# Kernel tuning notes

Hardware: AMD Instinct MI355X
Metric: run time of the kernel (lower is better)

## Reference

```python
import jax, jax.numpy as jnp
import numpy as np

B = 256
NO_A, NF_A = 64, 4   # class A: n_obj, n_field (all state fields)
NO_B, NF_B = 32, 3   # class B
NS = NF_A + NF_B     # total state fields = 7
DIN, DL, DG, DH = 128, 64, 64, 256
DGE = DG * NF_A + DG * NF_B          # 448 global encoding dim
DIN_A = DGE + DL * NF_A              # 704 decoder input dim, class A
DIN_B = DGE + DL * NF_B              # 640 decoder input dim, class B
NP = 2  # distribution params per field (mean, scale)


def lrelu(x):
    return jnp.where(x >= 0, x, 0.01 * x)


def setup_inputs() -> dict:
    key = jax.random.key(0)
    ks = iter(jax.random.split(key, 40))
    def rn(shape, s=1.0):
        return jax.random.normal(next(ks), shape, jnp.float32) * s
    def w(shape):
        return rn(shape, 0.05)
    def rb(shape):
        return jax.random.randint(next(ks), shape, 0, 2).astype(bool)
    inp = dict(
        x_A=rn((B, NO_A, NF_A, DIN)),
        x_B=rn((B, NO_B, NF_B, DIN)),
        global_mask=rb((B, NS, NF_A + NF_B)),
        local_mask_A=rb((B, NF_A, NF_A)),
        local_mask_B=rb((B, NF_B, NF_B)),
        objmask_A=rb((B, NO_A)),
        objmask_B=rb((B, NO_B)),
        enc_Wl_A=w((DIN, DL)), enc_bl_A=w((DL,)),
        enc_Wg_A=w((DIN, DG)), enc_bg_A=w((DG,)),
        enc_Wl_B=w((DIN, DL)), enc_bl_B=w((DL,)),
        enc_Wg_B=w((DIN, DG)), enc_bg_B=w((DG,)),
        dec_W1_A=w((NF_A, DIN_A, DH)), dec_b1_A=w((NF_A, DH)),
        dec_W2_A=w((NF_A, DH, DH)), dec_b2_A=w((NF_A, DH)),
        dec_Wp_A=w((NF_A, DH, NP)), dec_bp_A=w((NF_A, NP)),
        dec_W1_B=w((NF_B, DIN_B, DH)), dec_b1_B=w((NF_B, DH)),
        dec_W2_B=w((NF_B, DH, DH)), dec_b2_B=w((NF_B, DH)),
        dec_Wp_B=w((NF_B, DH, NP)), dec_bp_B=w((NF_B, NP)),
        rw_W1=w((DGE, DH)), rw_b1=w((DH,)),
        rw_W2=w((DH, DH)), rw_b2=w((DH,)),
        rw_W3=w((DH, 1)), rw_b3=w((1,)),
    )
    return inp


def encode_local(x, Wl, bl, attrmask):
    # x: (B, O, F, DIN) -> (B, O, S, F*DL), masked_retain over attrmask (B, S, F)
    h = jax.nn.relu(x @ Wl + bl)                                  # (B,O,F,DL)
    y = jnp.where(attrmask[:, None, :, :, None], h[:, :, None, :, :], 0.0)  # (B,O,S,F,DL)
    return y.reshape(y.shape[0], y.shape[1], y.shape[2], -1)


def encode_global(x, Wg, bg, attrmask, objmask):
    # x: (B, O, F, DIN), attrmask: (B, NS, F), objmask: (B, O)
    h = x @ Wg + bg                                               # (B,O,F,DG)
    h = jnp.where(objmask[:, :, None, None], h, 0.0)
    r = jax.nn.relu(jnp.sum(h, axis=1))                           # (B,F,DG) sum-pool over objects
    y = jnp.where(attrmask[:, :, :, None], r[:, None], 0.0)       # (B,NS,F,DG)
    y = jnp.concatenate([y, r[:, None]], axis=1)                  # (B,NS+1,F,DG)
    return y.reshape(y.shape[0], y.shape[1], -1)


def decode(x, W1, b1, W2, b2, Wp, bp):
    # x: (B, O, S, Din); per-field (s) decoders stacked on leading axis
    h = lrelu(jnp.einsum('bosi,sid->bosd', x, W1) + b1)
    h = lrelu(jnp.einsum('bosd,sde->bose', h, W2) + b2)
    return jnp.einsum('bose,sep->bosp', h, Wp) + bp               # (B,O,S,NP)


def reference(x_A, x_B, global_mask, local_mask_A, local_mask_B, objmask_A, objmask_B,
              enc_Wl_A, enc_bl_A, enc_Wg_A, enc_bg_A,
              enc_Wl_B, enc_bl_B, enc_Wg_B, enc_bg_B,
              dec_W1_A, dec_b1_A, dec_W2_A, dec_b2_A, dec_Wp_A, dec_bp_A,
              dec_W1_B, dec_b1_B, dec_W2_B, dec_b2_B, dec_Wp_B, dec_bp_B,
              rw_W1, rw_b1, rw_W2, rw_b2, rw_W3, rw_b3):
    g_A = encode_global(x_A, enc_Wg_A, enc_bg_A, global_mask[:, :, :NF_A], objmask_A)
    g_B = encode_global(x_B, enc_Wg_B, enc_bg_B, global_mask[:, :, NF_A:], objmask_B)
    G = jnp.concatenate([g_A, g_B], axis=2)                       # (B, NS+1, DGE)

    l_A = encode_local(x_A, enc_Wl_A, enc_bl_A, local_mask_A)     # (B,NO_A,NF_A,NF_A*DL)
    gs_A = jnp.broadcast_to(G[:, None, :NF_A, :], (B, NO_A, NF_A, DGE))
    out_A = decode(jnp.concatenate([l_A, gs_A], axis=3),
                   dec_W1_A, dec_b1_A, dec_W2_A, dec_b2_A, dec_Wp_A, dec_bp_A)

    l_B = encode_local(x_B, enc_Wl_B, enc_bl_B, local_mask_B)
    gs_B = jnp.broadcast_to(G[:, None, NF_A:NS, :], (B, NO_B, NF_B, DGE))
    out_B = decode(jnp.concatenate([l_B, gs_B], axis=3),
                   dec_W1_B, dec_b1_B, dec_W2_B, dec_b2_B, dec_Wp_B, dec_bp_B)

    h = lrelu(G[:, -1, :] @ rw_W1 + rw_b1)
    h = lrelu(h @ rw_W2 + rw_b2)
    reward = (h @ rw_W3 + rw_b3)[:, 0]                            # (B,)
    return out_A, out_B, reward
```

## Files before the change

kernel.cpp:

```cpp
#include <hip/hip_runtime.h>
#include <hip/hip_bf16.h>

constexpr int Bn   = 256;
constexpr int NOA  = 64, NFA = 4;
constexpr int NOB  = 32, NFB = 3;
constexpr int NS   = 7;
constexpr int DIN  = 128, DL = 64, DG = 64, DH = 256;
constexpr int DGE  = 448;
constexpr int DINA = 704;
constexpr int DINB = 640;

typedef short  short8v __attribute__((ext_vector_type(8)));
typedef float  f32x4   __attribute__((ext_vector_type(4)));

__device__ __forceinline__ unsigned short f2bf(float x) {
  union { float f; unsigned int u; } a; a.f = x;
  unsigned int r = a.u + 0x7fff + ((a.u >> 16) & 1);
  return (unsigned short)(r >> 16);
}


struct MidArgs {
  const float *xA, *xB, *WlA, *WlB, *blA, *blB;
  unsigned short *hlA, *hlB;
  const int *omA, *omB;
  const float *WgA, *bgA, *WgB, *bgB;
  float *rA, *rB;
  const float *W1A, *W1B, *W2A, *W2B;
  unsigned short *W1tA, *W1tB, *W1gtA, *W1gtB, *W2tA, *W2tB;
};

template<int F>
__device__ void hl_body(const float* __restrict__ x, const float* __restrict__ Wl,
                        const float* __restrict__ bl, unsigned short* __restrict__ hlf,
                        int m0, unsigned char* smem) {
  auto Asb = reinterpret_cast<unsigned short(*)[72]>(smem);
  auto Bsb = reinterpret_cast<unsigned short(*)[136]>(smem + 36864);
  float (*tile)[65] = reinterpret_cast<float(*)[65]>(smem);
  const int t = threadIdx.x, w = t >> 6, lane = t & 63;
  const int lr = lane & 15, lg = lane >> 4;
  constexpr int KB1 = 2 * F;

#pragma unroll
  for (int i = 0; i < 32; ++i) {
    int idx = t + i * 256;
    tile[idx >> 6][idx & 63] = Wl[idx];
  }
  __syncthreads();
#pragma unroll
  for (int i = 0; i < 32; ++i) {
    int idx = t + i * 256;
    int n = idx >> 7, k = idx & 127;
    Bsb[n][k] = f2bf(tile[k][n]);
  }
  __syncthreads();

  f32x4 acc[4][4] = {};
  for (int k0 = 0; k0 < DIN; k0 += 64) {
    const float* xp = x + (size_t)(m0 + t) * DIN + k0;
#pragma unroll
    for (int j = 0; j < 8; ++j) {
      float4 a = *(const float4*)(xp + j * 8);
      float4 b = *(const float4*)(xp + j * 8 + 4);
      union { short8v v; unsigned short e[8]; } u;
      u.e[0] = f2bf(a.x); u.e[1] = f2bf(a.y); u.e[2] = f2bf(a.z); u.e[3] = f2bf(a.w);
      u.e[4] = f2bf(b.x); u.e[5] = f2bf(b.y); u.e[6] = f2bf(b.z); u.e[7] = f2bf(b.w);
      *reinterpret_cast<short8v*>(&Asb[t][j * 8]) = u.v;
    }
#pragma unroll
    for (int ks = 0; ks < 2; ++ks) {
      short8v af[4], bf[4];
#pragma unroll
      for (int mi = 0; mi < 4; ++mi)
        af[mi] = *reinterpret_cast<const short8v*>(&Asb[w * 64 + mi * 16 + lr][ks * 32 + lg * 8]);
#pragma unroll
      for (int ni = 0; ni < 4; ++ni)
        bf[ni] = *reinterpret_cast<const short8v*>(&Bsb[ni * 16 + lr][k0 + ks * 32 + lg * 8]);
#pragma unroll
      for (int mi = 0; mi < 4; ++mi)
#pragma unroll
        for (int ni = 0; ni < 4; ++ni)
          acc[mi][ni] = __builtin_amdgcn_mfma_f32_16x16x32_bf16(
              af[mi], bf[ni], acc[mi][ni], 0, 0, 0);
    }
  }
#pragma unroll
  for (int mi = 0; mi < 4; ++mi)
#pragma unroll
    for (int ni = 0; ni < 4; ++ni)
#pragma unroll
      for (int reg = 0; reg < 4; ++reg) {
        int row = mi * 16 + lg * 4 + reg;
        int col = ni * 16 + lr;
        float v = fmaxf(acc[mi][ni][reg] + bl[col], 0.f);
        Asb[w * 64 + row][col] = f2bf(v);
      }
  const int mpb = m0 + w * 64;
#pragma unroll
  for (int j = 0; j < 8; ++j) {
    int c = lane + j * 64;
    int ml = c >> 3, dls = c & 7;
    int mp = mpb + ml;
    int mrow = mp / F, f = mp % F;
    int m6 = mrow >> 6, mi = (mrow >> 4) & 3, lr2 = mrow & 15;
    int kb = 2 * f + (dls >> 2), lg2 = dls & 3;
    size_t dst = ((((size_t)m6 * KB1 + kb) * 4 + mi) * 64 + (lg2 * 16 + lr2)) * 8;
    *reinterpret_cast<short8v*>(hlf + dst) =
        *reinterpret_cast<const short8v*>(&Asb[w * 64 + ml][dls * 8]);
  }
}

template<int O, int F>
__device__ void xsum_rg_body(const float* __restrict__ x, const int* __restrict__ om,
                             const float* __restrict__ Wg, const float* __restrict__ bg,
                             float* __restrict__ r, int b, unsigned char* smem) {
  float* xsm = reinterpret_cast<float*>(smem + 36864 + 17408);
  const int t = threadIdx.x, f = t >> 6, lane = t & 63;
  if (f >= F) return;
  unsigned long long bal = __ballot(lane < O && om[(size_t)b * O + lane] != 0);
  float cnt = (float)__popcll(bal);
  float a0 = 0.f, a1 = 0.f;
  const float* xb = x + ((size_t)b * O * F + f) * DIN + lane;
#pragma unroll 8
  for (int o = 0; o < O; ++o) {
    float m = (float)((bal >> o) & 1ull);
    a0 += m * xb[(size_t)o * F * DIN];
    a1 += m * xb[(size_t)o * F * DIN + 64];
  }
  xsm[f * 128 + lane] = a0;
  xsm[f * 128 + lane + 64] = a1;
  asm volatile("s_waitcnt lgkmcnt(0)" ::: "memory");
  float acc = 0.f;
  const float* wp = Wg + lane;
#pragma unroll 8
  for (int i = 0; i < DIN; ++i) acc += xsm[f * 128 + i] * wp[(size_t)i * DG];
  acc += cnt * bg[lane];
  r[((size_t)b * F + f) * DG + lane] = fmaxf(acc, 0.f);
}

__device__ void wtrans_tile(const float* __restrict__ src, unsigned short* __restrict__ dst,
                            int N, int DINc, int koff, int Kout,
                            int s, int kt, int nt, unsigned char* smem) {
  float (*tile)[65] = reinterpret_cast<float(*)[65]>(smem);
  const int t = threadIdx.x;
#pragma unroll
  for (int i = 0; i < 16; ++i) {
    int rr = (t >> 6) + i * 4, c = t & 63;
    tile[rr][c] = src[((size_t)s * DINc + koff + kt * 64 + rr) * N + nt * 64 + c];
  }
  __syncthreads();
#pragma unroll
  for (int i = 0; i < 2; ++i) {
    int cidx = t + i * 256;
    int n = cidx >> 3, kc = (cidx & 7) * 8;
    union { short8v v; unsigned short e[8]; } u;
#pragma unroll
    for (int j = 0; j < 8; ++j) u.e[j] = f2bf(tile[kc + j][n]);
    *reinterpret_cast<short8v*>(dst + ((size_t)s * N + nt * 64 + n) * Kout + kt * 64 + kc) = u.v;
  }
}

__device__ void wtrans_frag(const float* __restrict__ src, unsigned short* __restrict__ dst,
                            int DINc, int koff, int KB,
                            int s, int kt, int nt, unsigned char* smem) {
  float (*tile)[65] = reinterpret_cast<float(*)[65]>(smem);
  const int t = threadIdx.x;
#pragma unroll
  for (int i = 0; i < 16; ++i) {
    int rr = (t >> 6) + i * 4, c = t & 63;
    tile[rr][c] = src[((size_t)s * DINc + koff + kt * 64 + rr) * 256 + nt * 64 + c];
  }
  __syncthreads();
#pragma unroll
  for (int i = 0; i < 2; ++i) {
    int cidx = t + i * 256;
    int nl = cidx >> 3, kslot = cidx & 7;
    union { short8v v; unsigned short e[8]; } u;
#pragma unroll
    for (int j = 0; j < 8; ++j) u.e[j] = f2bf(tile[kslot * 8 + j][nl]);
    int kb = kt * 2 + (kslot >> 2);
    int lane = (kslot & 3) * 16 + (nl & 15);
    int nchunk = nt * 4 + (nl >> 4);
    *reinterpret_cast<short8v*>(
        dst + ((((size_t)s * KB + kb) * 16 + nchunk) * 64 + lane) * 8) = u.v;
  }
}

__global__ __launch_bounds__(256) void mid_kernel(MidArgs a) {
  __shared__ __align__(16) unsigned char smem[56320];
  const int bid = blockIdx.x;
  if (bid < 256) {
    hl_body<NFA>(a.xA, a.WlA, a.blA, a.hlA, bid * 256, smem);
    xsum_rg_body<NOA, NFA>(a.xA, a.omA, a.WgA, a.bgA, a.rA, bid, smem);
  } else if (bid < 352) {
    hl_body<NFB>(a.xB, a.WlB, a.blB, a.hlB, (bid - 256) * 256, smem);
  } else if (bid < 608) {
    xsum_rg_body<NOB, NFB>(a.xB, a.omB, a.WgB, a.bgB, a.rB, bid - 352, smem);
  } else {
    int r = bid - 608;
    if (r < 64)       { wtrans_frag(a.W1A, a.W1tA, DINA, 0, 8,
                                    r / 16, (r % 16) >> 2, r & 3, smem); }
    else if (r < 100) { r -= 64;  wtrans_frag(a.W1B, a.W1tB, DINB, 0, 6,
                                    r / 12, (r % 12) >> 2, r & 3, smem); }
    else if (r < 212) { r -= 100; wtrans_tile(a.W1A, a.W1gtA, 256, DINA, NFA * DL, DGE,
                                    r / 28, (r % 28) >> 2, r & 3, smem); }
    else if (r < 296) { r -= 212; wtrans_tile(a.W1B, a.W1gtB, 256, DINB, NFB * DL, DGE,
                                    r / 28, (r % 28) >> 2, r & 3, smem); }
    else if (r < 360) { r -= 296; wtrans_frag(a.W2A, a.W2tA, DH, 0, 8,
                                    r / 16, (r % 16) >> 2, r & 3, smem); }
    else              { r -= 360; wtrans_frag(a.W2B, a.W2tB, DH, 0, 8,
                                    r / 16, (r % 16) >> 2, r & 3, smem); }
  }
}

struct GprArgs {
  const float *rA, *rB; const int *gm;
  const unsigned short *W1gtA, *W1gtB;
  const float *b1A, *b1B;
  float *g1A, *g1B;
  const float *rwW1, *rwb1, *rwW2, *rwb2, *rwW3, *rwb3;
  float *outR;
};

__device__ void gpart_body(const GprArgs& a, int bx, int sg, unsigned char* smem) {
  auto Asb = reinterpret_cast<unsigned short(*)[72]>(smem);
  auto Bsb = reinterpret_cast<unsigned short(*)[72]>(smem + 9216);
  const int t = threadIdx.x, w = t >> 6, lane = t & 63;
  const int lr = lane & 15, lg = lane >> 4;
  const int m0 = bx * 64;
  const unsigned short* W1gt; const float* b1; float* g1; int S, sl;
  if (sg < NFA) { W1gt = a.W1gtA; b1 = a.b1A; g1 = a.g1A; S = NFA; sl = sg; }
  else          { W1gt = a.W1gtB; b1 = a.b1B; g1 = a.g1B; S = NFB; sl = sg - NFA; }

  f32x4 acc[4][4] = {};
  for (int kt = 0; kt < 7; ++kt) {
    __syncthreads();
    const int f = kt;
    const float* rsrc = (f < NFA) ? (a.rA + (size_t)f * DG) : (a.rB + (size_t)(f - NFA) * DG);
    const int rstride = (f < NFA) ? NFA * DG : NFB * DG;
#pragma unroll
    for (int i = 0; i < 2; ++i) {
      int c = t + i * 256;
      int row = c >> 3, kc = (c & 7) * 8;
      int b = m0 + row;
      float mk = (a.gm[((size_t)b * NS + sg) * NS + f] != 0) ? 1.f : 0.f;
      const float* rp = rsrc + (size_t)b * rstride + kc;
      union { short8v v; unsigned short e[8]; } u;
#pragma unroll
      for (int j = 0; j < 8; ++j) u.e[j] = f2bf(mk * rp[j]);
      *reinterpret_cast<short8v*>(&Asb[row][kc]) = u.v;
    }
#pragma unroll
    for (int i = 0; i < 8; ++i) {
      int c = t + i * 256;
      int n = c >> 3, kc = (c & 7) * 8;
      *reinterpret_cast<short8v*>(&Bsb[n][kc]) = *reinterpret_cast<const short8v*>(
          W1gt + ((size_t)sl * 256 + n) * DGE + kt * 64 + kc);
    }
    __syncthreads();
#pragma unroll
    for (int ks = 0; ks < 2; ++ks) {
      short8v af[4], bf[4];
#pragma unroll
      for (int mi = 0; mi < 4; ++mi)
        af[mi] = *reinterpret_cast<const short8v*>(&Asb[mi * 16 + lr][ks * 32 + lg * 8]);
#pragma unroll
      for (int ni = 0; ni < 4; ++ni)
        bf[ni] = *reinterpret_cast<const short8v*>(&Bsb[w * 64 + ni * 16 + lr][ks * 32 + lg * 8]);
#pragma unroll
      for (int mi = 0; mi < 4; ++mi)
#pragma unroll
        for (int ni = 0; ni < 4; ++ni)
          acc[mi][ni] = __builtin_amdgcn_mfma_f32_16x16x32_bf16(
              af[mi], bf[ni], acc[mi][ni], 0, 0, 0);
    }
  }
#pragma unroll
  for (int mi = 0; mi < 4; ++mi)
#pragma unroll
    for (int reg = 0; reg < 4; ++reg) {
      int b = m0 + mi * 16 + lg * 4 + reg;
#pragma unroll
      for (int ni = 0; ni < 4; ++ni) {
        int col = w * 64 + ni * 16 + lr;
        g1[((size_t)b * S + sl) * DH + col] = acc[mi][ni][reg] + b1[(size_t)sl * DH + col];
      }
    }
}

__device__ void reward_body(const GprArgs& a, int b, unsigned char* smem) {
  float* Gs = reinterpret_cast<float*>(smem);
  float* h1 = Gs + DGE;
  float* red = h1 + DH;
  const int t = threadIdx.x;
  for (int j = t; j < DGE; j += 256)
    Gs[j] = (j < NFA * DG) ? a.rA[((size_t)b * NFA + (j >> 6)) * DG + (j & 63)]
                           : a.rB[((size_t)b * NFB + ((j - NFA * DG) >> 6)) * DG + (j & 63)];
  __syncthreads();
  float acc = a.rwb1[t];
  for (int j = 0; j < DGE; ++j) acc += Gs[j] * a.rwW1[(size_t)j * DH + t];
  h1[t] = (acc >= 0.f) ? acc : 0.01f * acc;
  __syncthreads();
  acc = a.rwb2[t];
  for (int j = 0; j < DH; ++j) acc += h1[j] * a.rwW2[(size_t)j * DH + t];
  acc = (acc >= 0.f) ? acc : 0.01f * acc;
  red[t] = acc * a.rwW3[t];
  __syncthreads();
  for (int off = 128; off > 0; off >>= 1) {
    if (t < off) red[t] += red[t + off];
    __syncthreads();
  }
  if (t == 0) a.outR[b] = red[0] + a.rwb3[0];
}

__global__ __launch_bounds__(256) void gpr_kernel(GprArgs a) {
  __shared__ __align__(16) unsigned char smem[46080];
  const int bid = blockIdx.x;
  if (bid < 28) gpart_body(a, bid & 3, bid >> 2, smem);
  else          reward_body(a, bid - 28, smem);
}

struct DecArgs {
  const unsigned short *hlA, *hlB, *W1tA, *W1tB, *W2tA, *W2tB;
  const int *lmA, *lmB;
  const float *g1A, *g1B, *WpA, *WpB, *b2A, *b2B, *bpA, *bpB;
  float *outA, *outB;
};

template<int NO, int F>
__device__ __forceinline__ void dec_body(
    int mt, int s, unsigned short* h1s , float* red ,
    const unsigned short* __restrict__ hlf, const int* __restrict__ lm,
    const float* __restrict__ g1,
    const unsigned short* __restrict__ W1f, const unsigned short* __restrict__ W2f,
    const float* __restrict__ Wp, const float* __restrict__ b2,
    const float* __restrict__ bp, float* __restrict__ out) {
  constexpr int KB1 = 2 * F;
  const int t = threadIdx.x, w = t >> 6, lane = t & 63;
  const int lr = lane & 15, lg = lane >> 4;
  const int mh = w >> 2, nq = w & 3;
  const int m6 = mt * 2 + mh;
  const int m0 = mt * 128;

  int mk0[F], mk1[F];
#pragma unroll
  for (int f = 0; f < F; ++f) {
    if (NO == 64) {
      mk0[f] = mk1[f] = lm[((size_t)m6 * F + s) * F + f];
    } else {
      int b0 = m6 * 2;
      mk0[f] = lm[((size_t)b0 * F + s) * F + f];
      mk1[f] = lm[((size_t)(b0 + 1) * F + s) * F + f];
    }
  }
  float g1r[2][4];
#pragma unroll
  for (int ni = 0; ni < 4; ++ni) {
    int col = nq * 64 + ni * 16 + lr;
    if (NO == 64) {
      g1r[0][ni] = g1[((size_t)m6 * F + s) * DH + col];
      g1r[1][ni] = g1r[0][ni];
    } else {
      g1r[0][ni] = g1[((size_t)(m6 * 2) * F + s) * DH + col];
      g1r[1][ni] = g1[((size_t)(m6 * 2 + 1) * F + s) * DH + col];
    }
  }

  f32x4 acc[4][4] = {};

  const unsigned short* Afb = hlf + (size_t)m6 * KB1 * 2048;
  const unsigned short* B1b = W1f + (size_t)s * KB1 * 8192 + (size_t)nq * 4 * 512;
#pragma unroll
  for (int f = 0; f < F; ++f) {
    if ((mk0[f] | mk1[f]) == 0) continue;
#pragma unroll
    for (int sub = 0; sub < 2; ++sub) {
      int kb = 2 * f + sub;
      short8v af[4], bf[4];
      const unsigned short* ab = Afb + (size_t)kb * 2048 + lane * 8;
#pragma unroll
      for (int mi = 0; mi < 4; ++mi)
        af[mi] = *reinterpret_cast<const short8v*>(ab + mi * 512);
      if (NO == 32) {
#pragma unroll
        for (int mi = 0; mi < 4; ++mi)
          if (!((mi < 2) ? mk0[f] : mk1[f])) af[mi] = short8v{0,0,0,0,0,0,0,0};
      }
      const unsigned short* bb = B1b + (size_t)kb * 8192 + lane * 8;
#pragma unroll
      for (int ni = 0; ni < 4; ++ni)
        bf[ni] = *reinterpret_cast<const short8v*>(bb + ni * 512);
#pragma unroll
      for (int mi = 0; mi < 4; ++mi)
#pragma unroll
        for (int ni = 0; ni < 4; ++ni)
          acc[mi][ni] = __builtin_amdgcn_mfma_f32_16x16x32_bf16(
              af[mi], bf[ni], acc[mi][ni], 0, 0, 0);
    }
  }

#pragma unroll
  for (int mi = 0; mi < 4; ++mi)
#pragma unroll
    for (int reg = 0; reg < 4; ++reg) {
      int row = mh * 64 + mi * 16 + lg * 4 + reg;
      int gi = (NO == 32) ? (mi >> 1) : 0;
#pragma unroll
      for (int ni = 0; ni < 4; ++ni) {
        int col = nq * 64 + ni * 16 + lr;
        float v = acc[mi][ni][reg] + g1r[gi][ni];
        v = (v >= 0.f) ? v : 0.01f * v;
        h1s[row * 264 + col] = f2bf(v);
        acc[mi][ni][reg] = 0.f;
      }
    }
  __syncthreads();

  const unsigned short* B2b = W2f + (size_t)s * 8 * 8192 + (size_t)nq * 4 * 512 + lane * 8;
#pragma unroll
  for (int kb = 0; kb < 8; ++kb) {
    short8v af[4], bf[4];
#pragma unroll
    for (int mi = 0; mi < 4; ++mi)
      af[mi] = *reinterpret_cast<const short8v*>(
          h1s + (mh * 64 + mi * 16 + lr) * 264 + kb * 32 + lg * 8);
#pragma unroll
    for (int ni = 0; ni < 4; ++ni)
      bf[ni] = *reinterpret_cast<const short8v*>(B2b + (size_t)kb * 8192 + ni * 512);
#pragma unroll
    for (int mi = 0; mi < 4; ++mi)
#pragma unroll
      for (int ni = 0; ni < 4; ++ni)
        acc[mi][ni] = __builtin_amdgcn_mfma_f32_16x16x32_bf16(
            af[mi], bf[ni], acc[mi][ni], 0, 0, 0);
  }

  float part[4][4][2] = {};
  const float* Wps = Wp + (size_t)s * DH * 2;
  const float* b2s = b2 + (size_t)s * DH;
#pragma unroll
  for (int ni = 0; ni < 4; ++ni) {
    int col = nq * 64 + ni * 16 + lr;
    float wp0 = Wps[col * 2 + 0], wp1 = Wps[col * 2 + 1], bb2 = b2s[col];
#pragma unroll
    for (int mi = 0; mi < 4; ++mi)
#pragma unroll
      for (int reg = 0; reg < 4; ++reg) {
        float v = acc[mi][ni][reg] + bb2;
        v = (v >= 0.f) ? v : 0.01f * v;
        part[mi][reg][0] += v * wp0;
        part[mi][reg][1] += v * wp1;
      }
  }
#pragma unroll
  for (int off = 1; off < 16; off <<= 1)
#pragma unroll
    for (int mi = 0; mi < 4; ++mi)
#pragma unroll
      for (int reg = 0; reg < 4; ++reg) {
        part[mi][reg][0] += __shfl_xor(part[mi][reg][0], off, 64);
        part[mi][reg][1] += __shfl_xor(part[mi][reg][1], off, 64);
      }
  if (lr == 0)
#pragma unroll
    for (int mi = 0; mi < 4; ++mi)
#pragma unroll
      for (int reg = 0; reg < 4; ++reg) {
        int rowin = mi * 16 + lg * 4 + reg;
        red[(w * 64 + rowin) * 2 + 0] = part[mi][reg][0];
        red[(w * 64 + rowin) * 2 + 1] = part[mi][reg][1];
      }
  __syncthreads();
  if (t < 256) {
    int row = t >> 1, p = t & 1;
    int mhr = row >> 6, rowin = row & 63;
    float sum = 0.f;
#pragma unroll
    for (int q = 0; q < 4; ++q)
      sum += red[((mhr * 4 + q) * 64 + rowin) * 2 + p];
    out[((size_t)(m0 + row) * F + s) * 2 + p] = sum + bp[(size_t)s * 2 + p];
  }
}

__global__ __launch_bounds__(512, 4) void dec_kernel(DecArgs a) {
  __shared__ __align__(16) unsigned short h1s[128 * 264];
  __shared__ float red[1024];
  const int bid = blockIdx.x;
  if (bid < 512) {
    dec_body<NOA, NFA>(bid & 127, bid >> 7, h1s, red, a.hlA, a.lmA, a.g1A,
                       a.W1tA, a.W2tA, a.WpA, a.b2A, a.bpA, a.outA);
  } else {
    int r = bid - 512;
    dec_body<NOB, NFB>(r & 63, r >> 6, h1s, red, a.hlB, a.lmB, a.g1B,
                       a.W1tB, a.W2tB, a.WpB, a.b2B, a.bpB, a.outB);
  }
}

extern "C" void kernel_launch(void* const* d_in, const int* in_sizes, int n_in,
                              void* d_out, int out_size, void* d_ws, size_t ws_size,
                              hipStream_t stream) {
  const float* x_A  = (const float*)d_in[0];
  const float* x_B  = (const float*)d_in[1];
  const int*   gm   = (const int*)d_in[2];
  const int*   lmA  = (const int*)d_in[3];
  const int*   lmB  = (const int*)d_in[4];
  const int*   omA  = (const int*)d_in[5];
  const int*   omB  = (const int*)d_in[6];
  const float* Wl_A = (const float*)d_in[7];
  const float* bl_A = (const float*)d_in[8];
  const float* Wg_A = (const float*)d_in[9];
  const float* bg_A = (const float*)d_in[10];
  const float* Wl_B = (const float*)d_in[11];
  const float* bl_B = (const float*)d_in[12];
  const float* Wg_B = (const float*)d_in[13];
  const float* bg_B = (const float*)d_in[14];
  const float* W1_A = (const float*)d_in[15];
  const float* b1_A = (const float*)d_in[16];
  const float* W2_A = (const float*)d_in[17];
  const float* b2_A = (const float*)d_in[18];
  const float* Wp_A = (const float*)d_in[19];
  const float* bp_A = (const float*)d_in[20];
  const float* W1_B = (const float*)d_in[21];
  const float* b1_B = (const float*)d_in[22];
  const float* W2_B = (const float*)d_in[23];
  const float* b2_B = (const float*)d_in[24];
  const float* Wp_B = (const float*)d_in[25];
  const float* bp_B = (const float*)d_in[26];
  const float* rwW1 = (const float*)d_in[27];
  const float* rwb1 = (const float*)d_in[28];
  const float* rwW2 = (const float*)d_in[29];
  const float* rwb2 = (const float*)d_in[30];
  const float* rwW3 = (const float*)d_in[31];
  const float* rwb3 = (const float*)d_in[32];

  float* ws   = (float*)d_ws;
  float* rA   = ws;
  float* rB   = rA + 65536;
  float* g1A  = rB + 49152;
  float* g1B  = g1A + 262144;
  unsigned short* us    = (unsigned short*)(g1B + 196608);
  unsigned short* hlA   = us;
  unsigned short* hlB   = hlA + 4194304;
  unsigned short* W1tA  = hlB + 1572864;
  unsigned short* W1tB  = W1tA + 262144;
  unsigned short* W2tA  = W1tB + 147456;
  unsigned short* W2tB  = W2tA + 262144;
  unsigned short* W1gtA = W2tB + 196608;
  unsigned short* W1gtB = W1gtA + 458752;

  float* outA = (float*)d_out;
  float* outB = outA + 131072;
  float* outR = outA + 180224;

  MidArgs m;
  m.xA = x_A; m.xB = x_B; m.WlA = Wl_A; m.WlB = Wl_B; m.blA = bl_A; m.blB = bl_B;
  m.hlA = hlA; m.hlB = hlB; m.omA = omA; m.omB = omB;
  m.WgA = Wg_A; m.bgA = bg_A; m.WgB = Wg_B; m.bgB = bg_B;
  m.rA = rA; m.rB = rB;
  m.W1A = W1_A; m.W1B = W1_B; m.W2A = W2_A; m.W2B = W2_B;
  m.W1tA = W1tA; m.W1tB = W1tB; m.W1gtA = W1gtA; m.W1gtB = W1gtB;
  m.W2tA = W2tA; m.W2tB = W2tB;

  GprArgs g;
  g.rA = rA; g.rB = rB; g.gm = gm; g.W1gtA = W1gtA; g.W1gtB = W1gtB;
  g.b1A = b1_A; g.b1B = b1_B; g.g1A = g1A; g.g1B = g1B;
  g.rwW1 = rwW1; g.rwb1 = rwb1; g.rwW2 = rwW2; g.rwb2 = rwb2;
  g.rwW3 = rwW3; g.rwb3 = rwb3; g.outR = outR;

  DecArgs d;
  d.hlA = hlA; d.hlB = hlB; d.W1tA = W1tA; d.W1tB = W1tB;
  d.W2tA = W2tA; d.W2tB = W2tB; d.lmA = lmA; d.lmB = lmB;
  d.g1A = g1A; d.g1B = g1B; d.WpA = Wp_A; d.WpB = Wp_B;
  d.b2A = b2_A; d.b2B = b2_B; d.bpA = bp_A; d.bpB = bp_B;
  d.outA = outA; d.outB = outB;

  mid_kernel<<<1016, 256, 0, stream>>>(m);
  gpr_kernel<<<284, 256, 0, stream>>>(g);
  dec_kernel<<<704, 512, 0, stream>>>(d);
}
```

Before: 82.69 us.

## Halve decoder block M-tile and add L2 prewarm of local encodings

```diff
diff --git a/kernel.cpp b/kernel.cpp
--- a/kernel.cpp
+++ b/kernel.cpp
@@ -220,7 +220,17 @@
   float *g1A, *g1B;
   const float *rwW1, *rwb1, *rwW2, *rwb2, *rwW3, *rwb3;
   float *outR;
+  const unsigned short *hlA, *hlB;
 };
+
+__device__ void warm_body(const unsigned short* __restrict__ p, int n16) {
+  const int4* q = reinterpret_cast<const int4*>(p);
+  const int t = threadIdx.x;
+  for (int i = 0; i < n16; ++i) {
+    int4 v = q[t + i * 256];
+    asm volatile("" :: "v"(v.x), "v"(v.y), "v"(v.z), "v"(v.w));
+  }
+}
 
 __device__ void gpart_body(const GprArgs& a, int bx, int sg, unsigned char* smem) {
   auto Asb = reinterpret_cast<unsigned short(*)[72]>(smem);
@@ -316,8 +326,10 @@
 __global__ __launch_bounds__(256) void gpr_kernel(GprArgs a) {
   __shared__ __align__(16) unsigned char smem[46080];
   const int bid = blockIdx.x;
-  if (bid < 28) gpart_body(a, bid & 3, bid >> 2, smem);
-  else          reward_body(a, bid - 28, smem);
+  if (bid < 256)      warm_body(a.hlA + (size_t)bid * 16384, 8);
+  else if (bid < 384) warm_body(a.hlB + (size_t)(bid - 256) * 12288, 6);
+  else if (bid < 412) gpart_body(a, (bid - 384) & 3, (bid - 384) >> 2, smem);
+  else                reward_body(a, bid - 412, smem);
 }
 
 struct DecArgs {
@@ -329,7 +341,7 @@
 
 template<int NO, int F>
 __device__ __forceinline__ void dec_body(
-    int mt, int s, unsigned short* h1s , float* red ,
+    int m6, int s, unsigned short* h1s , float* red ,
     const unsigned short* __restrict__ hlf, const int* __restrict__ lm,
     const float* __restrict__ g1,
     const unsigned short* __restrict__ W1f, const unsigned short* __restrict__ W2f,
@@ -338,115 +350,115 @@
   constexpr int KB1 = 2 * F;
   const int t = threadIdx.x, w = t >> 6, lane = t & 63;
   const int lr = lane & 15, lg = lane >> 4;
-  const int mh = w >> 2, nq = w & 3;
-  const int m6 = mt * 2 + mh;
-  const int m0 = mt * 128;
-
-  int mk0[F], mk1[F];
+  const int m0 = m6 * 64;
+
+  int mk0 = 0, mk1 = 0;
+  if (NO == 64) {
+#pragma unroll
+    for (int f = 0; f < F; ++f)
+      if (lm[((size_t)m6 * F + s) * F + f]) mk0 |= 1 << f;
+    mk1 = mk0;
+  } else {
+    int b0 = m6 * 2;
+#pragma unroll
+    for (int f = 0; f < F; ++f) {
+      if (lm[((size_t)b0 * F + s) * F + f])       mk0 |= 1 << f;
+      if (lm[((size_t)(b0 + 1) * F + s) * F + f]) mk1 |= 1 << f;
+    }
+  }
+  float g1r[2][2];
+#pragma unroll
+  for (int n2 = 0; n2 < 2; ++n2) {
+    int col = w * 32 + n2 * 16 + lr;
+    if (NO == 64) {
+      g1r[0][n2] = g1[((size_t)m6 * F + s) * DH + col];
+      g1r[1][n2] = g1r[0][n2];
+    } else {
+      g1r[0][n2] = g1[((size_t)(m6 * 2) * F + s) * DH + col];
+      g1r[1][n2] = g1[((size_t)(m6 * 2 + 1) * F + s) * DH + col];
+    }
+  }
+
+  f32x4 acc[4][2] = {};
+
 #pragma unroll
   for (int f = 0; f < F; ++f) {
-    if (NO == 64) {
-      mk0[f] = mk1[f] = lm[((size_t)m6 * F + s) * F + f];
-    } else {
-      int b0 = m6 * 2;
-      mk0[f] = lm[((size_t)b0 * F + s) * F + f];
-      mk1[f] = lm[((size_t)(b0 + 1) * F + s) * F + f];
-    }
-  }
-  float g1r[2][4];
-#pragma unroll
-  for (int ni = 0; ni < 4; ++ni) {
-    int col = nq * 64 + ni * 16 + lr;
-    if (NO == 64) {
-      g1r[0][ni] = g1[((size_t)m6 * F + s) * DH + col];
-      g1r[1][ni] = g1r[0][ni];
-    } else {
-      g1r[0][ni] = g1[((size_t)(m6 * 2) * F + s) * DH + col];
-      g1r[1][ni] = g1[((size_t)(m6 * 2 + 1) * F + s) * DH + col];
-    }
-  }
-
-  f32x4 acc[4][4] = {};
-
-  const unsigned short* Afb = hlf + (size_t)m6 * KB1 * 2048;
-  const unsigned short* B1b = W1f + (size_t)s * KB1 * 8192 + (size_t)nq * 4 * 512;
-#pragma unroll
-  for (int f = 0; f < F; ++f) {
-    if ((mk0[f] | mk1[f]) == 0) continue;
+    if (!(((mk0 | mk1) >> f) & 1)) continue;
 #pragma unroll
     for (int sub = 0; sub < 2; ++sub) {
       int kb = 2 * f + sub;
-      short8v af[4], bf[4];
-      const unsigned short* ab = Afb + (size_t)kb * 2048 + lane * 8;
+      const unsigned short* ab = hlf + (((size_t)m6 * KB1 + kb) * 4) * 512 + lane * 8;
+      short8v af[4];
 #pragma unroll
       for (int mi = 0; mi < 4; ++mi)
         af[mi] = *reinterpret_cast<const short8v*>(ab + mi * 512);
       if (NO == 32) {
-#pragma unroll
-        for (int mi = 0; mi < 4; ++mi)
-          if (!((mi < 2) ? mk0[f] : mk1[f])) af[mi] = short8v{0,0,0,0,0,0,0,0};
-      }
-      const unsigned short* bb = B1b + (size_t)kb * 8192 + lane * 8;
-#pragma unroll
-      for (int ni = 0; ni < 4; ++ni)
-        bf[ni] = *reinterpret_cast<const short8v*>(bb + ni * 512);
+        if (!((mk0 >> f) & 1)) { af[0] = short8v{0,0,0,0,0,0,0,0}; af[1] = af[0]; }
+        if (!((mk1 >> f) & 1)) { af[2] = short8v{0,0,0,0,0,0,0,0}; af[3] = af[2]; }
+      }
+      const unsigned short* bb =
+          W1f + (((size_t)s * KB1 + kb) * 16 + w * 2) * 512 + lane * 8;
+      short8v bf[2];
+      bf[0] = *reinterpret_cast<const short8v*>(bb);
+      bf[1] = *reinterpret_cast<const short8v*>(bb + 512);
 #pragma unroll
       for (int mi = 0; mi < 4; ++mi)
 #pragma unroll
-        for (int ni = 0; ni < 4; ++ni)
-          acc[mi][ni] = __builtin_amdgcn_mfma_f32_16x16x32_bf16(
-              af[mi], bf[ni], acc[mi][ni], 0, 0, 0);
-    }
-  }
-
-#pragma unroll
-  for (int mi = 0; mi < 4; ++mi)
+        for (int n2 = 0; n2 < 2; ++n2)
+          acc[mi][n2] = __builtin_amdgcn_mfma_f32_16x16x32_bf16(
+              af[mi], bf[n2], acc[mi][n2], 0, 0, 0);
+    }
+  }
+
+#pragma unroll
+  for (int mi = 0; mi < 4; ++mi) {
+    int gi = (NO == 32) ? (mi >> 1) : 0;
 #pragma unroll
     for (int reg = 0; reg < 4; ++reg) {
-      int row = mh * 64 + mi * 16 + lg * 4 + reg;
-      int gi = (NO == 32) ? (mi >> 1) : 0;
-#pragma unroll
-      for (int ni = 0; ni < 4; ++ni) {
-        int col = nq * 64 + ni * 16 + lr;
-        float v = acc[mi][ni][reg] + g1r[gi][ni];
+      int row = mi * 16 + lg * 4 + reg;
+#pragma unroll
+      for (int n2 = 0; n2 < 2; ++n2) {
+        int col = w * 32 + n2 * 16 + lr;
+        float v = acc[mi][n2][reg] + g1r[gi][n2];
         v = (v >= 0.f) ? v : 0.01f * v;
         h1s[row * 264 + col] = f2bf(v);
-        acc[mi][ni][reg] = 0.f;
-      }
-    }
-  __syncthreads();
-
-  const unsigned short* B2b = W2f + (size_t)s * 8 * 8192 + (size_t)nq * 4 * 512 + lane * 8;
+        acc[mi][n2][reg] = 0.f;
+      }
+    }
+  }
+  __syncthreads();
+
 #pragma unroll
   for (int kb = 0; kb < 8; ++kb) {
-    short8v af[4], bf[4];
+    short8v af[4], bf[2];
 #pragma unroll
     for (int mi = 0; mi < 4; ++mi)
       af[mi] = *reinterpret_cast<const short8v*>(
-          h1s + (mh * 64 + mi * 16 + lr) * 264 + kb * 32 + lg * 8);
-#pragma unroll
-    for (int ni = 0; ni < 4; ++ni)
-      bf[ni] = *reinterpret_cast<const short8v*>(B2b + (size_t)kb * 8192 + ni * 512);
+          h1s + (mi * 16 + lr) * 264 + kb * 32 + lg * 8);
+    const unsigned short* bb =
+        W2f + (((size_t)s * 8 + kb) * 16 + w * 2) * 512 + lane * 8;
+    bf[0] = *reinterpret_cast<const short8v*>(bb);
+    bf[1] = *reinterpret_cast<const short8v*>(bb + 512);
 #pragma unroll
     for (int mi = 0; mi < 4; ++mi)
 #pragma unroll
-      for (int ni = 0; ni < 4; ++ni)
-        acc[mi][ni] = __builtin_amdgcn_mfma_f32_16x16x32_bf16(
-            af[mi], bf[ni], acc[mi][ni], 0, 0, 0);
+      for (int n2 = 0; n2 < 2; ++n2)
+        acc[mi][n2] = __builtin_amdgcn_mfma_f32_16x16x32_bf16(
+            af[mi], bf[n2], acc[mi][n2], 0, 0, 0);
   }
 
   float part[4][4][2] = {};
   const float* Wps = Wp + (size_t)s * DH * 2;
   const float* b2s = b2 + (size_t)s * DH;
 #pragma unroll
-  for (int ni = 0; ni < 4; ++ni) {
-    int col = nq * 64 + ni * 16 + lr;
+  for (int n2 = 0; n2 < 2; ++n2) {
+    int col = w * 32 + n2 * 16 + lr;
     float wp0 = Wps[col * 2 + 0], wp1 = Wps[col * 2 + 1], bb2 = b2s[col];
 #pragma unroll
     for (int mi = 0; mi < 4; ++mi)
 #pragma unroll
       for (int reg = 0; reg < 4; ++reg) {
-        float v = acc[mi][ni][reg] + bb2;
+        float v = acc[mi][n2][reg] + bb2;
         v = (v >= 0.f) ? v : 0.01f * v;
         part[mi][reg][0] += v * wp0;
         part[mi][reg][1] += v * wp1;
@@ -466,32 +478,30 @@
     for (int mi = 0; mi < 4; ++mi)
 #pragma unroll
       for (int reg = 0; reg < 4; ++reg) {
-        int rowin = mi * 16 + lg * 4 + reg;
-        red[(w * 64 + rowin) * 2 + 0] = part[mi][reg][0];
-        red[(w * 64 + rowin) * 2 + 1] = part[mi][reg][1];
-      }
-  __syncthreads();
-  if (t < 256) {
+        int row = mi * 16 + lg * 4 + reg;
+        red[((size_t)w * 64 + row) * 2 + 0] = part[mi][reg][0];
+        red[((size_t)w * 64 + row) * 2 + 1] = part[mi][reg][1];
+      }
+  __syncthreads();
+  if (t < 128) {
     int row = t >> 1, p = t & 1;
-    int mhr = row >> 6, rowin = row & 63;
     float sum = 0.f;
 #pragma unroll
-    for (int q = 0; q < 4; ++q)
-      sum += red[((mhr * 4 + q) * 64 + rowin) * 2 + p];
+    for (int q = 0; q < 8; ++q) sum += red[((size_t)q * 64 + row) * 2 + p];
     out[((size_t)(m0 + row) * F + s) * 2 + p] = sum + bp[(size_t)s * 2 + p];
   }
 }
 
-__global__ __launch_bounds__(512, 4) void dec_kernel(DecArgs a) {
-  __shared__ __align__(16) unsigned short h1s[128 * 264];
+__global__ __launch_bounds__(512, 6) void dec_kernel(DecArgs a) {
+  __shared__ __align__(16) unsigned short h1s[64 * 264];
   __shared__ float red[1024];
   const int bid = blockIdx.x;
-  if (bid < 512) {
-    dec_body<NOA, NFA>(bid & 127, bid >> 7, h1s, red, a.hlA, a.lmA, a.g1A,
+  if (bid < 1024) {
+    dec_body<NOA, NFA>(bid & 255, bid >> 8, h1s, red, a.hlA, a.lmA, a.g1A,
                        a.W1tA, a.W2tA, a.WpA, a.b2A, a.bpA, a.outA);
   } else {
-    int r = bid - 512;
-    dec_body<NOB, NFB>(r & 63, r >> 6, h1s, red, a.hlB, a.lmB, a.g1B,
+    int r = bid - 1024;
+    dec_body<NOB, NFB>(r & 127, r >> 7, h1s, red, a.hlB, a.lmB, a.g1B,
                        a.W1tB, a.W2tB, a.WpB, a.b2B, a.bpB, a.outB);
   }
 }
@@ -566,6 +576,7 @@
   g.b1A = b1_A; g.b1B = b1_B; g.g1A = g1A; g.g1B = g1B;
   g.rwW1 = rwW1; g.rwb1 = rwb1; g.rwW2 = rwW2; g.rwb2 = rwb2;
   g.rwW3 = rwW3; g.rwb3 = rwb3; g.outR = outR;
+  g.hlA = hlA; g.hlB = hlB;
 
   DecArgs d;
   d.hlA = hlA; d.hlB = hlB; d.W1tA = W1tA; d.W1tB = W1tB;
@@ -575,6 +586,6 @@
   d.outA = outA; d.outB = outB;
 
   mid_kernel<<<1016, 256, 0, stream>>>(m);
-  gpr_kernel<<<284, 256, 0, stream>>>(g);
-  dec_kernel<<<704, 512, 0, stream>>>(d);
-}
+  gpr_kernel<<<668, 256, 0, stream>>>(g);
+  dec_kernel<<<1408, 512, 0, stream>>>(d);
+}
```

Result: slower. 97.21 us (+17.6%).

## Prefetch decoder activations into per-XCD L2 and make decoder masking branchless

Applied to the files above, without the earlier changes.

```diff
diff --git a/kernel.cpp b/kernel.cpp
--- a/kernel.cpp
+++ b/kernel.cpp
@@ -220,7 +220,17 @@
   float *g1A, *g1B;
   const float *rwW1, *rwb1, *rwW2, *rwb2, *rwW3, *rwb3;
   float *outR;
+  const unsigned short *hlA, *hlB;
 };
+
+__device__ void warm_body(const unsigned short* __restrict__ p, int n16) {
+  const int4* q = reinterpret_cast<const int4*>(p);
+  const int t = threadIdx.x;
+  for (int i = 0; i < n16; ++i) {
+    int4 v = q[t + i * 256];
+    asm volatile("" :: "v"(v.x), "v"(v.y), "v"(v.z), "v"(v.w));
+  }
+}
 
 __device__ void gpart_body(const GprArgs& a, int bx, int sg, unsigned char* smem) {
   auto Asb = reinterpret_cast<unsigned short(*)[72]>(smem);
@@ -316,8 +326,20 @@
 __global__ __launch_bounds__(256) void gpr_kernel(GprArgs a) {
   __shared__ __align__(16) unsigned char smem[46080];
   const int bid = blockIdx.x;
-  if (bid < 28) gpart_body(a, bid & 3, bid >> 2, smem);
-  else          reward_body(a, bid - 28, smem);
+  if (bid < 256) {
+    int xcd = bid & 7, idx = bid >> 3;
+    int m6 = (idx >> 1) * 16 + xcd * 2 + (idx & 1);
+    warm_body(a.hlA + (size_t)m6 * 16384, 8);
+  } else if (bid < 384) {
+    int local = bid - 256;
+    int xcd = local & 7, idx = local >> 3;
+    int m6 = (idx >> 1) * 16 + xcd * 2 + (idx & 1);
+    warm_body(a.hlB + (size_t)m6 * 12288, 6);
+  } else if (bid < 412) {
+    gpart_body(a, (bid - 384) & 3, (bid - 384) >> 2, smem);
+  } else {
+    reward_body(a, bid - 412, smem);
+  }
 }
 
 struct DecArgs {
@@ -342,15 +364,16 @@
   const int m6 = mt * 2 + mh;
   const int m0 = mt * 128;
 
-  int mk0[F], mk1[F];
+  unsigned mkl = 0, mkh = 0;
 #pragma unroll
   for (int f = 0; f < F; ++f) {
     if (NO == 64) {
-      mk0[f] = mk1[f] = lm[((size_t)m6 * F + s) * F + f];
+      unsigned bit = (lm[((size_t)m6 * F + s) * F + f] != 0) ? 1u : 0u;
+      mkl |= bit << f; mkh |= bit << f;
     } else {
       int b0 = m6 * 2;
-      mk0[f] = lm[((size_t)b0 * F + s) * F + f];
-      mk1[f] = lm[((size_t)(b0 + 1) * F + s) * F + f];
+      if (lm[((size_t)b0 * F + s) * F + f])       mkl |= 1u << f;
+      if (lm[((size_t)(b0 + 1) * F + s) * F + f]) mkh |= 1u << f;
     }
   }
   float g1r[2][4];
@@ -367,44 +390,40 @@
   }
 
   f32x4 acc[4][4] = {};
-
-  const unsigned short* Afb = hlf + (size_t)m6 * KB1 * 2048;
-  const unsigned short* B1b = W1f + (size_t)s * KB1 * 8192 + (size_t)nq * 4 * 512;
-#pragma unroll
-  for (int f = 0; f < F; ++f) {
-    if ((mk0[f] | mk1[f]) == 0) continue;
-#pragma unroll
-    for (int sub = 0; sub < 2; ++sub) {
-      int kb = 2 * f + sub;
-      short8v af[4], bf[4];
-      const unsigned short* ab = Afb + (size_t)kb * 2048 + lane * 8;
-#pragma unroll
-      for (int mi = 0; mi < 4; ++mi)
-        af[mi] = *reinterpret_cast<const short8v*>(ab + mi * 512);
-      if (NO == 32) {
-#pragma unroll
-        for (int mi = 0; mi < 4; ++mi)
-          if (!((mi < 2) ? mk0[f] : mk1[f])) af[mi] = short8v{0,0,0,0,0,0,0,0};
-      }
-      const unsigned short* bb = B1b + (size_t)kb * 8192 + lane * 8;
+  const short8v zero8 = {0, 0, 0, 0, 0, 0, 0, 0};
+
+  const unsigned short* Afb = hlf + (size_t)m6 * KB1 * 2048 + lane * 8;
+  const unsigned short* B1b = W1f + ((size_t)s * KB1 * 16 + nq * 4) * 512 + lane * 8;
+#pragma unroll
+  for (int kb = 0; kb < KB1; ++kb) {
+    const int f = kb >> 1;
+    short8v af[4], bf[4];
+#pragma unroll
+    for (int mi = 0; mi < 4; ++mi)
+      af[mi] = *reinterpret_cast<const short8v*>(Afb + (size_t)kb * 2048 + mi * 512);
+    const bool bl = (mkl >> f) & 1, bh = (mkh >> f) & 1;
+#pragma unroll
+    for (int mi = 0; mi < 4; ++mi) {
+      const bool ok = (mi < 2) ? bl : bh;
+      af[mi] = ok ? af[mi] : zero8;
+    }
+#pragma unroll
+    for (int ni = 0; ni < 4; ++ni)
+      bf[ni] = *reinterpret_cast<const short8v*>(B1b + (size_t)kb * 8192 + ni * 512);
+#pragma unroll
+    for (int mi = 0; mi < 4; ++mi)
 #pragma unroll
       for (int ni = 0; ni < 4; ++ni)
-        bf[ni] = *reinterpret_cast<const short8v*>(bb + ni * 512);
-#pragma unroll
-      for (int mi = 0; mi < 4; ++mi)
-#pragma unroll
-        for (int ni = 0; ni < 4; ++ni)
-          acc[mi][ni] = __builtin_amdgcn_mfma_f32_16x16x32_bf16(
-              af[mi], bf[ni], acc[mi][ni], 0, 0, 0);
-    }
-  }
-
-#pragma unroll
-  for (int mi = 0; mi < 4; ++mi)
+        acc[mi][ni] = __builtin_amdgcn_mfma_f32_16x16x32_bf16(
+            af[mi], bf[ni], acc[mi][ni], 0, 0, 0);
+  }
+
+#pragma unroll
+  for (int mi = 0; mi < 4; ++mi) {
+    int gi = (NO == 32) ? (mi >> 1) : 0;
 #pragma unroll
     for (int reg = 0; reg < 4; ++reg) {
       int row = mh * 64 + mi * 16 + lg * 4 + reg;
-      int gi = (NO == 32) ? (mi >> 1) : 0;
 #pragma unroll
       for (int ni = 0; ni < 4; ++ni) {
         int col = nq * 64 + ni * 16 + lr;
@@ -414,9 +433,10 @@
         acc[mi][ni][reg] = 0.f;
       }
     }
-  __syncthreads();
-
-  const unsigned short* B2b = W2f + (size_t)s * 8 * 8192 + (size_t)nq * 4 * 512 + lane * 8;
+  }
+  __syncthreads();
+
+  const unsigned short* B2b = W2f + ((size_t)s * 8 * 16 + nq * 4) * 512 + lane * 8;
 #pragma unroll
   for (int kb = 0; kb < 8; ++kb) {
     short8v af[4], bf[4];
@@ -467,8 +487,8 @@
 #pragma unroll
       for (int reg = 0; reg < 4; ++reg) {
         int rowin = mi * 16 + lg * 4 + reg;
-        red[(w * 64 + rowin) * 2 + 0] = part[mi][reg][0];
-        red[(w * 64 + rowin) * 2 + 1] = part[mi][reg][1];
+        red[((size_t)w * 64 + rowin) * 2 + 0] = part[mi][reg][0];
+        red[((size_t)w * 64 + rowin) * 2 + 1] = part[mi][reg][1];
       }
   __syncthreads();
   if (t < 256) {
@@ -477,7 +497,7 @@
     float sum = 0.f;
 #pragma unroll
     for (int q = 0; q < 4; ++q)
-      sum += red[((mhr * 4 + q) * 64 + rowin) * 2 + p];
+      sum += red[((size_t)(mhr * 4 + q) * 64 + rowin) * 2 + p];
     out[((size_t)(m0 + row) * F + s) * 2 + p] = sum + bp[(size_t)s * 2 + p];
   }
 }
@@ -566,6 +586,7 @@
   g.b1A = b1_A; g.b1B = b1_B; g.g1A = g1A; g.g1B = g1B;
   g.rwW1 = rwW1; g.rwb1 = rwb1; g.rwW2 = rwW2; g.rwb2 = rwb2;
   g.rwW3 = rwW3; g.rwb3 = rwb3; g.outR = outR;
+  g.hlA = hlA; g.hlB = hlB;
 
   DecArgs d;
   d.hlA = hlA; d.hlB = hlB; d.W1tA = W1tA; d.W1tB = W1tB;
@@ -575,6 +596,6 @@
   d.outA = outA; d.outB = outB;
 
   mid_kernel<<<1016, 256, 0, stream>>>(m);
-  gpr_kernel<<<284, 256, 0, stream>>>(g);
+  gpr_kernel<<<668, 256, 0, stream>>>(g);
   dec_kernel<<<704, 512, 0, stream>>>(d);
 }
```

New measurement: 94.42 us. 14.2% more time.
